# Performance work log

Hardware: AMD Instinct MI355X
Metric: run time of the kernel (lower is better)

## Reference

```python
import jax, jax.numpy as jnp
import numpy as np

INV_TEMP = 20.0
THRESHOLD = 0.01
SING_CUTOFF = 3.0
D0 = 128  # order-0 descriptor block
EPS = 1e-6


def setup_inputs() -> dict:
    key = jax.random.key(0)
    ks = jax.random.split(key, 6)
    B, N, M, D = 4, 4096, 4096, 256
    K = (D - D0) // 2
    return {
        "keypoints_A": jax.random.uniform(ks[0], (B, N, 2), jnp.float32) * 2.0 - 1.0,
        "descriptions_A": jax.random.normal(ks[1], (B, N, D), jnp.float32),
        "keypoints_B": jax.random.uniform(ks[2], (B, M, 2), jnp.float32) * 2.0 - 1.0,
        "descriptions_B": jax.random.normal(ks[3], (B, M, D), jnp.float32),
        "W_lstsq": jax.random.normal(ks[4], (D0, K), jnp.float32) * 0.1,
        "b_lstsq": jnp.zeros((K,), jnp.float32),
    }


def _svdvals_2x2(A):
    # singular values of [..,2,2] via eigenvalues of A^T A (closed form)
    M = jnp.einsum('...ki,...kj->...ij', A, A)
    t = M[..., 0, 0] + M[..., 1, 1]
    d = M[..., 0, 0] * M[..., 1, 1] - M[..., 0, 1] * M[..., 1, 0]
    disc = jnp.sqrt(jnp.maximum(0.25 * t * t - d, 0.0))
    lam_hi = 0.5 * t + disc
    lam_lo = jnp.maximum(0.5 * t - disc, 0.0)
    return jnp.sqrt(lam_hi), jnp.sqrt(lam_lo)


def reference(keypoints_A, descriptions_A, keypoints_B, descriptions_B, W_lstsq, b_lstsq):
    B, N, D = descriptions_A.shape
    K = (D - D0) // 2
    # --- dual softmax matcher (normalize=True) ---
    dA = descriptions_A / jnp.linalg.norm(descriptions_A, axis=-1, keepdims=True)
    dB = descriptions_B / jnp.linalg.norm(descriptions_B, axis=-1, keepdims=True)
    sim = INV_TEMP * jnp.einsum('bnd,bmd->bnm', dA, dB)  # [B,N,M]
    P = jax.nn.softmax(sim, axis=-2) * jax.nn.softmax(sim, axis=-1)
    # --- mutual nearest neighbors, fixed-shape (one candidate per A-row) ---
    j = jnp.argmax(P, axis=-1)  # [B,N]
    Pij = jnp.take_along_axis(P, j[..., None], axis=-1)[..., 0]
    colmax_j = jnp.take_along_axis(P.max(axis=-2), j, axis=-1)
    valid = (Pij >= colmax_j) & (Pij > THRESHOLD)  # mutual max + threshold
    # --- gather raw descriptors for matched pairs ---
    descB_m = jnp.take_along_axis(descriptions_B, j[..., None], axis=1)  # [B,N,D]
    desc0_A, desc1_A = descriptions_A[..., :D0], descriptions_A[..., D0:]
    desc0_B, desc1_B = descB_m[..., :D0], descB_m[..., D0:]
    # --- lstsq weights from order-0 features ---
    wA = jax.nn.softplus(desc0_A @ W_lstsq + b_lstsq)
    wB = jax.nn.softplus(desc0_B @ W_lstsq + b_lstsq)
    w = jnp.sqrt(wA * wB)  # [B,N,K]
    # --- weighted 2x2 affine lstsq: A x ~ y ---
    X = desc1_A.reshape(B, N, K, 2)
    Y = desc1_B.reshape(B, N, K, 2)
    G = jnp.einsum('bnk,bnki,bnkj->bnij', w, X, X) + EPS * jnp.eye(2, dtype=X.dtype)
    C = jnp.einsum('bnk,bnki,bnkj->bnij', w, Y, X)
    est = jnp.swapaxes(jnp.linalg.solve(G, jnp.swapaxes(C, -1, -2)), -1, -2)  # [B,N,2,2]
    # --- singular value / determinant filter ---
    s_hi, s_lo = _svdvals_2x2(est)
    good = jnp.isfinite(s_hi + s_lo) & (s_hi < SING_CUTOFF) & (s_lo > 1.0 / SING_CUTOFF)
    det = est[..., 0, 0] * est[..., 1, 1] - est[..., 0, 1] * est[..., 1, 0]
    good = good & (det > 0)  # remove_negative_determinants=True
    valid = valid & good
    matches_A = keypoints_A  # row i of A pairs with column j[b,i]
    matches_B = jnp.take_along_axis(keypoints_B, j[..., None], axis=1)
    return matches_A, matches_B, j, valid
```

## Files before the change

kernel.cpp:

```cpp
#include <hip/hip_runtime.h>
#include <math.h>

#define Bb   4
#define Nn   4096
#define Mm   4096
#define Dd   256
#define D0c  128
#define Kc   64

typedef _Float16 half8 __attribute__((ext_vector_type(8)));
typedef float    f32x4 __attribute__((ext_vector_type(4)));

__device__ __forceinline__ unsigned encf(float f) {
    unsigned u = __float_as_uint(f);
    return (u & 0x80000000u) ? ~u : (u | 0x80000000u);
}
__device__ __forceinline__ float decf(unsigned u) {
    return (u & 0x80000000u) ? __uint_as_float(u ^ 0x80000000u) : __uint_as_float(~u);
}
__device__ __forceinline__ float softplusf(float x) {
    return fmaxf(x, 0.f) + log1pf(expf(-fabsf(x)));
}
__device__ __forceinline__ void gl_lds16(const _Float16* g, _Float16* l) {
    __builtin_amdgcn_global_load_lds((const __attribute__((address_space(1))) void*)g,
                                     (__attribute__((address_space(3))) void*)l, 16, 0, 0);
}

__global__ __launch_bounds__(256) void prep_kernel(
    const float* __restrict__ dA, const float* __restrict__ dB,
    _Float16* __restrict__ Ah, _Float16* __restrict__ Al,
    _Float16* __restrict__ Bh, _Float16* __restrict__ Bl)
{
    const int t = threadIdx.x, wave = t >> 6, lane = t & 63;
    const int row = blockIdx.x * 4 + wave;
    const float* src = blockIdx.y ? dB : dA;
    _Float16* dh = blockIdx.y ? Bh : Ah;
    _Float16* dl = blockIdx.y ? Bl : Al;
    const float4 v = *(const float4*)&src[(size_t)row * Dd + lane * 4];
    float ss = v.x * v.x + v.y * v.y + v.z * v.z + v.w * v.w;
#pragma unroll
    for (int m = 32; m; m >>= 1) ss += __shfl_xor(ss, m, 64);
    const float inv = 1.0f / sqrtf(ss);
    float x[4] = {v.x * inv, v.y * inv, v.z * inv, v.w * inv};
    union { _Float16 h[4]; uint2 u; } ph, pl;
#pragma unroll
    for (int i = 0; i < 4; i++) {
        _Float16 h = (_Float16)x[i];
        ph.h[i] = h;
        pl.h[i] = (_Float16)((x[i] - (float)h) * 4096.f);
    }
    const size_t toff = (size_t)(row >> 7) * 32768
                      + (size_t)(lane >> 3) * 4096
                      + (size_t)((lane >> 1) & 3) * 1024
                      + (size_t)(row & 127) * 8 + (lane & 1) * 4;
    *(uint2*)&dh[toff] = ph.u;
    *(uint2*)&dl[toff] = pl.u;
}

template<int PB, int STORE>
__global__ __launch_bounds__(256, 2) void sim_kernel(
    const _Float16* __restrict__ Ah, const _Float16* __restrict__ Al,
    const _Float16* __restrict__ Bh, const _Float16* __restrict__ Bl,
    const float* __restrict__ Lrow_g, const float* __restrict__ Lcol_g,
    float* __restrict__ rowsumP, float* __restrict__ colsumP,
    float* __restrict__ rkey, int* __restrict__ rmArr, float* __restrict__ rcvArr,
    unsigned* __restrict__ cmU, float* __restrict__ simG, int b0)
{
    __shared__ _Float16 lds[2][4][4][128][8];
    __shared__ float    colp[128];
    __shared__ unsigned colu[128];
    __shared__ float    shL[128], shLc[128];

    const int t = threadIdx.x;
    const int wave = t >> 6, lane = t & 63;
    const int mt = blockIdx.x, nt = blockIdx.y, bbl = blockIdx.z;
    const int bb = b0 + bbl;
    const int n0 = nt * 128, m0 = mt * 128;

    if (PB) {
        if (t < 128) {
            shL[t]  = Lrow_g[bb * Nn + n0 + t];
            shLc[t] = Lcol_g[bb * Mm + m0 + t];
            colu[t] = 0u;
        }
    } else {
        if (t < 128) colp[t] = 0.f;
    }

    const _Float16* gb;
    {
        const size_t offA = (size_t)(bb * Nn + n0) * Dd;
        const size_t offB = (size_t)(bb * Mm + m0) * Dd;
        if      (wave == 0) gb = Ah + offA;
        else if (wave == 1) gb = Al + offA;
        else if (wave == 2) gb = Bh + offB;
        else                gb = Bl + offB;
    }

    f32x4 acc1[2][8], acc2[2][8];
#pragma unroll
    for (int ti = 0; ti < 2; ti++)
#pragma unroll
        for (int tj = 0; tj < 8; tj++) { acc1[ti][tj] = (f32x4)0.f; acc2[ti][tj] = (f32x4)0.f; }

    const int quad = lane >> 4, l15 = lane & 15;
    _Float16* lw0 = &lds[0][wave][0][0][0];
    _Float16* lw1 = &lds[1][wave][0][0][0];

#pragma unroll
    for (int q = 0; q < 8; ++q)
        gl_lds16(gb + q * 512 + lane * 8, lw0 + q * 512);

#pragma unroll
    for (int kc8 = 0; kc8 < 8; ++kc8) {
        const int cur = kc8 & 1;
        if (kc8 < 7) {
            _Float16* nw = cur ? lw0 : lw1;
            const _Float16* gsrc = gb + (kc8 + 1) * 4096;
#pragma unroll
            for (int q = 0; q < 8; ++q)
                gl_lds16(gsrc + q * 512 + lane * 8, nw + q * 512);
            asm volatile("s_waitcnt vmcnt(8)" ::: "memory");
        } else {
            asm volatile("s_waitcnt vmcnt(0)" ::: "memory");
        }
        __builtin_amdgcn_s_barrier();
        __builtin_amdgcn_sched_barrier(0);

        half8 afh[2], afl[2];
        afh[0] = *(const half8*)&lds[cur][0][quad][wave * 32 + l15][0];
        afh[1] = *(const half8*)&lds[cur][0][quad][wave * 32 + 16 + l15][0];
        afl[0] = *(const half8*)&lds[cur][1][quad][wave * 32 + l15][0];
        afl[1] = *(const half8*)&lds[cur][1][quad][wave * 32 + 16 + l15][0];
#pragma unroll
        for (int tj = 0; tj < 8; ++tj) {
            half8 bh = *(const half8*)&lds[cur][2][quad][tj * 16 + l15][0];
            half8 bl = *(const half8*)&lds[cur][3][quad][tj * 16 + l15][0];
#pragma unroll
            for (int ti = 0; ti < 2; ++ti) {
                acc1[ti][tj] = __builtin_amdgcn_mfma_f32_16x16x32_f16(afh[ti], bh, acc1[ti][tj], 0, 0, 0);
                acc2[ti][tj] = __builtin_amdgcn_mfma_f32_16x16x32_f16(afh[ti], bl, acc2[ti][tj], 0, 0, 0);
                acc2[ti][tj] = __builtin_amdgcn_mfma_f32_16x16x32_f16(afl[ti], bh, acc2[ti][tj], 0, 0, 0);
            }
        }
        asm volatile("s_waitcnt lgkmcnt(0)" ::: "memory");
        __builtin_amdgcn_s_barrier();
    }

    if (!PB) {
        float rp[8] = {0.f}, cp[8] = {0.f};
#pragma unroll
        for (int ti = 0; ti < 2; ++ti)
#pragma unroll
            for (int tj = 0; tj < 8; ++tj)
#pragma unroll
                for (int r = 0; r < 4; ++r) {
                    float dot = fmaf(acc2[ti][tj][r], 2.44140625e-4f, acc1[ti][tj][r]);
                    acc1[ti][tj][r] = dot;
                    float e = __expf(fmaf(20.f, dot, -20.f));
                    rp[ti * 4 + r] += e;
                    cp[tj] += e;
                }
#pragma unroll
        for (int i = 0; i < 8; ++i)
#pragma unroll
            for (int m = 1; m < 16; m <<= 1) rp[i] += __shfl_xor(rp[i], m, 64);
        if (l15 == 0) {
#pragma unroll
            for (int ti = 0; ti < 2; ++ti)
#pragma unroll
                for (int r = 0; r < 4; ++r)
                    rowsumP[(size_t)(bb * 32 + mt) * Nn + n0 + wave * 32 + ti * 16 + quad * 4 + r] = rp[ti * 4 + r];
        }
#pragma unroll
        for (int tj = 0; tj < 8; ++tj) {
            cp[tj] += __shfl_xor(cp[tj], 16, 64);
            cp[tj] += __shfl_xor(cp[tj], 32, 64);
        }
        if (quad == 0) {
#pragma unroll
            for (int tj = 0; tj < 8; ++tj) atomicAdd(&colp[tj * 16 + l15], cp[tj]);
        }
        __syncthreads();
        if (t < 128) colsumP[(size_t)(bb * 32 + nt) * Mm + m0 + t] = colp[t];
        if (STORE) {
            float* base = simG + ((size_t)bbl * Nn + n0) * Mm + m0;
#pragma unroll
            for (int ti = 0; ti < 2; ++ti)
#pragma unroll
                for (int r = 0; r < 4; ++r) {
                    float* rowp = base + (size_t)(wave * 32 + ti * 16 + quad * 4 + r) * Mm;
#pragma unroll
                    for (int tj = 0; tj < 8; ++tj)
                        __builtin_nontemporal_store(acc1[ti][tj][r], rowp + tj * 16 + l15);
                }
        }
    } else {
        float Lr[8];
#pragma unroll
        for (int ti = 0; ti < 2; ++ti)
#pragma unroll
            for (int r = 0; r < 4; ++r)
                Lr[ti * 4 + r] = shL[wave * 32 + ti * 16 + quad * 4 + r];

        float bk[8], bc[8];
        int bm[8];
        unsigned cu[8];
#pragma unroll
        for (int i = 0; i < 8; i++) { bk[i] = -INFINITY; bc[i] = -INFINITY; bm[i] = 0x7fffffff; }
#pragma unroll
        for (int j = 0; j < 8; j++) cu[j] = 0u;

#pragma unroll
        for (int ti = 0; ti < 2; ++ti)
#pragma unroll
            for (int tj = 0; tj < 8; ++tj)
#pragma unroll
                for (int r = 0; r < 4; ++r) {
                    float dot = fmaf(acc2[ti][tj][r], 2.44140625e-4f, acc1[ti][tj][r]);
                    float cv = fmaf(40.f, dot, -40.f - Lr[ti * 4 + r]);
                    float kv = cv - shLc[tj * 16 + l15];
                    const int i = ti * 4 + r;
                    if (kv > bk[i]) { bk[i] = kv; bm[i] = m0 + tj * 16 + l15; bc[i] = cv; }
                    unsigned e = encf(cv);
                    if (e > cu[tj]) cu[tj] = e;
                }
#pragma unroll
        for (int i = 0; i < 8; ++i) {
#pragma unroll
            for (int m = 1; m < 16; m <<= 1) {
                float okv = __shfl_xor(bk[i], m, 64);
                int   om  = __shfl_xor(bm[i], m, 64);
                float ocv = __shfl_xor(bc[i], m, 64);
                if (okv > bk[i] || (okv == bk[i] && om < bm[i])) { bk[i] = okv; bm[i] = om; bc[i] = ocv; }
            }
        }
        if (l15 == 0) {
#pragma unroll
            for (int ti = 0; ti < 2; ++ti)
#pragma unroll
                for (int r = 0; r < 4; ++r) {
                    const int i = ti * 4 + r;
                    size_t idx = (size_t)(bb * 32 + mt) * Nn + n0 + wave * 32 + ti * 16 + quad * 4 + r;
                    rkey[idx] = bk[i]; rmArr[idx] = bm[i]; rcvArr[idx] = bc[i];
                }
        }
#pragma unroll
        for (int tj = 0; tj < 8; ++tj) {
            unsigned o = __shfl_xor(cu[tj], 16, 64); if (o > cu[tj]) cu[tj] = o;
            o = __shfl_xor(cu[tj], 32, 64); if (o > cu[tj]) cu[tj] = o;
        }
        if (quad == 0) {
#pragma unroll
            for (int tj = 0; tj < 8; ++tj) atomicMax(&colu[tj * 16 + l15], cu[tj]);
        }
        __syncthreads();
        if (t < 128) cmU[(size_t)(bb * 32 + nt) * Mm + m0 + t] = colu[t];
    }
}

__global__ __launch_bounds__(256) void logsum_kernel(
    const float* __restrict__ rowsumP, const float* __restrict__ colsumP,
    float* __restrict__ Lrow, float* __restrict__ Lcol, int b0, int CB)
{
    int t = blockIdx.x * 256 + threadIdx.x;
    int half = CB * 4096;
    int which = t >= half;
    int idx = which ? (t - half) : t;
    int bb = b0 + (idx >> 12), n = idx & 4095;
    const float* P = which ? colsumP : rowsumP;
    float s = 0.f;
    for (int mt = 0; mt < 32; ++mt) s += P[(size_t)(bb * 32 + mt) * 4096 + n];
    (which ? Lcol : Lrow)[bb * 4096 + n] = logf(s);
}

__global__ __launch_bounds__(256) void scan_kernel(
    const float* __restrict__ simG,
    const float* __restrict__ Lrow, const float* __restrict__ Lcol,
    float* __restrict__ kvP, float* __restrict__ cvP, int* __restrict__ jP,
    unsigned* __restrict__ colPartU, int b0)
{
    __shared__ unsigned colu[1024];
    const int t = threadIdx.x, wave = t >> 6, lane = t & 63;
    const int blk = blockIdx.x;
    const int bbl = blk >> 9;
    const int r9 = blk & 511;
    const int stripe = r9 >> 2, q = r9 & 3;
    const int bb = b0 + bbl;
    const int col0 = q * 1024;
    const int row0 = stripe * 32 + wave * 8;

    for (int i = t; i < 1024; i += 256) colu[i] = 0u;
    __syncthreads();

    f32x4 Lc4[4], cmax[4];
    const float* LcB = Lcol + bb * Mm + col0;
#pragma unroll
    for (int c = 0; c < 4; ++c) {
        Lc4[c] = *(const f32x4*)&LcB[c * 256 + lane * 4];
        cmax[c] = (f32x4)(-INFINITY);
    }

    const float* rowbase = simG + (size_t)(bbl * Nn + row0) * Mm + col0;
    f32x4 cur[4], nxt[4];
#pragma unroll
    for (int c = 0; c < 4; ++c)
        cur[c] = __builtin_nontemporal_load((const f32x4*)&rowbase[c * 256 + lane * 4]);

    for (int r = 0; r < 8; ++r) {
        if (r < 7) {
            const float* nrow = rowbase + (size_t)(r + 1) * Mm;
#pragma unroll
            for (int c = 0; c < 4; ++c)
                nxt[c] = __builtin_nontemporal_load((const f32x4*)&nrow[c * 256 + lane * 4]);
        }
        const int n = bb * Nn + row0 + r;
        const float Ln = Lrow[n];
        const float cbias = -40.f - Ln;
        float bk = -INFINITY, bc = -INFINITY;
        int bm = 0x7fffffff;
#pragma unroll
        for (int c = 0; c < 4; ++c) {
            float cv0 = fmaf(40.f, cur[c].x, cbias);
            float cv1 = fmaf(40.f, cur[c].y, cbias);
            float cv2 = fmaf(40.f, cur[c].z, cbias);
            float cv3 = fmaf(40.f, cur[c].w, cbias);
            cmax[c].x = fmaxf(cmax[c].x, cv0);
            cmax[c].y = fmaxf(cmax[c].y, cv1);
            cmax[c].z = fmaxf(cmax[c].z, cv2);
            cmax[c].w = fmaxf(cmax[c].w, cv3);
            const int mb = col0 + c * 256 + lane * 4;
            float kv0 = cv0 - Lc4[c].x;
            float kv1 = cv1 - Lc4[c].y;
            float kv2 = cv2 - Lc4[c].z;
            float kv3 = cv3 - Lc4[c].w;
            if (kv0 > bk) { bk = kv0; bm = mb;     bc = cv0; }
            if (kv1 > bk) { bk = kv1; bm = mb + 1; bc = cv1; }
            if (kv2 > bk) { bk = kv2; bm = mb + 2; bc = cv2; }
            if (kv3 > bk) { bk = kv3; bm = mb + 3; bc = cv3; }
        }
#pragma unroll
        for (int sh = 1; sh < 64; sh <<= 1) {
            float okv = __shfl_xor(bk, sh, 64);
            int   om  = __shfl_xor(bm, sh, 64);
            float ocv = __shfl_xor(bc, sh, 64);
            if (okv > bk || (okv == bk && om < bm)) { bk = okv; bm = om; bc = ocv; }
        }
        if (lane == 0) {
            size_t o = ((size_t)bb * Nn + row0 + r) * 4 + q;
            kvP[o] = bk; cvP[o] = bc; jP[o] = bm;
        }
#pragma unroll
        for (int c = 0; c < 4; ++c) cur[c] = nxt[c];
    }
#pragma unroll
    for (int c = 0; c < 4; ++c) {
        const int mb = c * 256 + lane * 4;
        atomicMax(&colu[mb],     encf(cmax[c].x));
        atomicMax(&colu[mb + 1], encf(cmax[c].y));
        atomicMax(&colu[mb + 2], encf(cmax[c].z));
        atomicMax(&colu[mb + 3], encf(cmax[c].w));
    }
    __syncthreads();
    unsigned* cp = colPartU + (size_t)blk * 1024;
    for (int i = t; i < 1024; i += 256) cp[i] = colu[i];
}

__global__ __launch_bounds__(256) void colreduce_kernel(
    const unsigned* __restrict__ colPartU, float* __restrict__ colMaxF, int b0)
{
    const int tid = blockIdx.x * 256 + threadIdx.x;
    const int bbl = tid >> 12;
    const int m = tid & 4095;
    const int q = m >> 10, ml = m & 1023;
    unsigned mx = 0u;
    for (int s = 0; s < 128; ++s) {
        unsigned v = colPartU[((size_t)(bbl * 512 + s * 4 + q)) * 1024 + ml];
        if (v > mx) mx = v;
    }
    colMaxF[(size_t)(b0 + bbl) * Mm + m] = decf(mx);
}

__global__ __launch_bounds__(256) void validate_kernel(
    const float* __restrict__ kvP, const float* __restrict__ cvP,
    const int* __restrict__ jP, const float* __restrict__ colMaxF,
    float* __restrict__ outJ, int* __restrict__ jIdx, int* __restrict__ v1)
{
    const float LOG_THR = -4.605170185988091f;
    const int p = blockIdx.x * 256 + threadIdx.x;
    const int bb = p >> 12;
    float bk = -INFINITY, bc = -INFINITY;
    int bm = 0x7fffffff;
#pragma unroll
    for (int q = 0; q < 4; ++q) {
        size_t o = (size_t)p * 4 + q;
        float k = kvP[o];
        int   m = jP[o];
        if (k > bk || (k == bk && m < bm)) { bk = k; bm = m; bc = cvP[o]; }
    }
    const float cm = colMaxF[(size_t)bb * Mm + bm];
    const int ok = (bk > LOG_THR) && (bc >= cm);
    outJ[p] = (float)bm;
    jIdx[p] = bm;
    v1[p] = ok;
}

__global__ __launch_bounds__(256) void finalize_kernel(
    const float* __restrict__ rkey, const int* __restrict__ rmArr,
    const float* __restrict__ rcvArr, const unsigned* __restrict__ cmU,
    float* __restrict__ outJ, int* __restrict__ jIdx, int* __restrict__ v1)
{
    const float LOG_THR = -4.605170185988091f;
    int p = blockIdx.x * 256 + threadIdx.x;
    int bb = p >> 12, n = p & 4095;
    float bk = -INFINITY, bc = -INFINITY;
    int bm = 0;
    for (int mt = 0; mt < 32; ++mt) {
        size_t idx = (size_t)(bb * 32 + mt) * Nn + n;
        float k = rkey[idx];
        if (k > bk) { bk = k; bm = rmArr[idx]; bc = rcvArr[idx]; }
    }
    unsigned u = 0u;
    for (int nt = 0; nt < 32; ++nt) {
        unsigned c = cmU[(size_t)(bb * 32 + nt) * Mm + bm];
        if (c > u) u = c;
    }
    float cm = decf(u);
    int ok = (bk > LOG_THR) && (bc >= cm);
    outJ[p] = (float)bm;
    jIdx[p] = bm;
    v1[p]   = ok;
}

__global__ __launch_bounds__(256) void affine_kernel(
    const float* __restrict__ descA, const float* __restrict__ descB,
    const float* __restrict__ kpA, const float* __restrict__ kpB,
    const float* __restrict__ W, const float* __restrict__ bvec,
    const int* __restrict__ jIdx, const int* __restrict__ v1,
    float* __restrict__ outA, float* __restrict__ outB, float* __restrict__ outV)
{
    __shared__ float Ws[D0c * Kc];
    __shared__ float sbuf[4][4][D0c];
    const int t = threadIdx.x, wave = t >> 6, lane = t & 63;
    for (int i = t; i < D0c * Kc; i += 256) Ws[i] = W[i];
    const float bl = bvec[lane];
    __syncthreads();

    float* s0A = sbuf[wave][0];
    float* s1A = sbuf[wave][1];
    float* s0B = sbuf[wave][2];
    float* s1B = sbuf[wave][3];

    for (int p = 0; p < 8; ++p) {
        const int point = blockIdx.x * 32 + wave * 8 + p;
        const int bb = point >> 12;
        const int j = jIdx[point];
        const float* da = descA + (size_t)point * Dd;
        const float* db = descB + (size_t)(bb * Mm + j) * Dd;
        s0A[lane] = da[lane];       s0A[64 + lane] = da[64 + lane];
        s1A[lane] = da[128 + lane]; s1A[64 + lane] = da[192 + lane];
        s0B[lane] = db[lane];       s0B[64 + lane] = db[64 + lane];
        s1B[lane] = db[128 + lane]; s1B[64 + lane] = db[192 + lane];
        __syncthreads();

        float xa = bl, xb = bl;
#pragma unroll 8
        for (int d = 0; d < 128; ++d) {
            float w_ = Ws[d * 64 + lane];
            xa = fmaf(s0A[d], w_, xa);
            xb = fmaf(s0B[d], w_, xb);
        }
        float wa = softplusf(xa), wb = softplusf(xb);
        float w = sqrtf(wa * wb);
        float x0 = s1A[2 * lane], x1 = s1A[2 * lane + 1];
        float y0 = s1B[2 * lane], y1 = s1B[2 * lane + 1];
        float g00 = w * x0 * x0, g01 = w * x0 * x1, g11 = w * x1 * x1;
        float c00 = w * y0 * x0, c01 = w * y0 * x1;
        float c10 = w * y1 * x0, c11 = w * y1 * x1;
#pragma unroll
        for (int m = 32; m; m >>= 1) {
            g00 += __shfl_xor(g00, m, 64); g01 += __shfl_xor(g01, m, 64); g11 += __shfl_xor(g11, m, 64);
            c00 += __shfl_xor(c00, m, 64); c01 += __shfl_xor(c01, m, 64);
            c10 += __shfl_xor(c10, m, 64); c11 += __shfl_xor(c11, m, 64);
        }
        if (lane == 0) {
            g00 += 1e-6f; g11 += 1e-6f;
            float det = g00 * g11 - g01 * g01;
            float e00 = (c00 * g11 - c01 * g01) / det;
            float e01 = (c01 * g00 - c00 * g01) / det;
            float e10 = (c10 * g11 - c11 * g01) / det;
            float e11 = (c11 * g00 - c10 * g01) / det;
            float m00 = e00 * e00 + e10 * e10;
            float m01 = e00 * e01 + e10 * e11;
            float m11 = e01 * e01 + e11 * e11;
            float tr = m00 + m11;
            float dm = m00 * m11 - m01 * m01;
            float disc = sqrtf(fmaxf(0.25f * tr * tr - dm, 0.f));
            float lhi = 0.5f * tr + disc;
            float llo = fmaxf(0.5f * tr - disc, 0.f);
            float shi = sqrtf(lhi), slo = sqrtf(llo);
            float sdet = e00 * e11 - e01 * e10;
            int good = isfinite(shi + slo) && (shi < 3.0f) && (slo > 0.33333334f) && (sdet > 0.f);
            int valid = v1[point] && good;
            outA[2 * point]     = kpA[2 * point];
            outA[2 * point + 1] = kpA[2 * point + 1];
            const float* kb = kpB + (size_t)(bb * Mm + j) * 2;
            outB[2 * point]     = kb[0];
            outB[2 * point + 1] = kb[1];
            outV[point] = valid ? 1.f : 0.f;
        }
        __syncthreads();
    }
}

extern "C" void kernel_launch(void* const* d_in, const int* in_sizes, int n_in,
                              void* d_out, int out_size, void* d_ws, size_t ws_size,
                              hipStream_t stream) {
    const float* kpA = (const float*)d_in[0];
    const float* dA  = (const float*)d_in[1];
    const float* kpB = (const float*)d_in[2];
    const float* dB  = (const float*)d_in[3];
    const float* W   = (const float*)d_in[4];
    const float* bl  = (const float*)d_in[5];
    float* out = (float*)d_out;

    char* ws = (char*)d_ws;
    _Float16* Ah = (_Float16*)ws;  ws += 8388608;
    _Float16* Al = (_Float16*)ws;  ws += 8388608;
    _Float16* Bh = (_Float16*)ws;  ws += 8388608;
    _Float16* Bl = (_Float16*)ws;  ws += 8388608;
    float*    rowsumP = (float*)ws;    ws += 2097152;
    float*    colsumP = (float*)ws;    ws += 2097152;
    float*    Lrow    = (float*)ws;    ws += 65536;
    float*    Lcol    = (float*)ws;    ws += 65536;
    int*      jIdx    = (int*)ws;      ws += 65536;
    int*      v1      = (int*)ws;      ws += 65536;
    float*    kvP     = (float*)ws;    ws += 262144;
    float*    cvP     = (float*)ws;    ws += 262144;
    int*      jP      = (int*)ws;      ws += 262144;
    float*    colMaxF = (float*)ws;    ws += 65536;
    char*     big     = ws;

    const size_t base = (size_t)(big - (char*)d_ws);

    float*    rkey  = (float*)big;
    int*      rmArr = (int*)(big + 2097152);
    float*    rcvArr= (float*)(big + 4194304);
    unsigned* cmU   = (unsigned*)(big + 6291456);

    float* outA = out;
    float* outB = out + 32768;
    float* outJ = out + 65536;
    float* outV = out + 81920;

    const size_t per = 67108864ull + 2097152ull;
    int CB = 0;
    if      (ws_size >= base + 2 * per) CB = 2;
    else if (ws_size >= base + 1 * per) CB = 1;

    prep_kernel<<<dim3(4096, 2), 256, 0, stream>>>(dA, dB, Ah, Al, Bh, Bl);

    if (CB) {
        float*    simG     = (float*)big;
        unsigned* colPartU = (unsigned*)(big + (size_t)CB * 67108864);
        for (int b0 = 0; b0 < Bb; b0 += CB) {
            sim_kernel<0, 1><<<dim3(32, 32, CB), 256, 0, stream>>>(
                Ah, Al, Bh, Bl, nullptr, nullptr, rowsumP, colsumP,
                nullptr, nullptr, nullptr, nullptr, simG, b0);
            logsum_kernel<<<32 * CB, 256, 0, stream>>>(rowsumP, colsumP, Lrow, Lcol, b0, CB);
            scan_kernel<<<512 * CB, 256, 0, stream>>>(simG, Lrow, Lcol, kvP, cvP, jP, colPartU, b0);
            colreduce_kernel<<<16 * CB, 256, 0, stream>>>(colPartU, colMaxF, b0);
        }
        validate_kernel<<<64, 256, 0, stream>>>(kvP, cvP, jP, colMaxF, outJ, jIdx, v1);
    } else {
        sim_kernel<0, 0><<<dim3(32, 32, Bb), 256, 0, stream>>>(
            Ah, Al, Bh, Bl, nullptr, nullptr, rowsumP, colsumP,
            nullptr, nullptr, nullptr, nullptr, nullptr, 0);
        logsum_kernel<<<32 * Bb, 256, 0, stream>>>(rowsumP, colsumP, Lrow, Lcol, 0, Bb);
        sim_kernel<1, 0><<<dim3(32, 32, Bb), 256, 0, stream>>>(
            Ah, Al, Bh, Bl, Lrow, Lcol, nullptr, nullptr,
            rkey, rmArr, rcvArr, cmU, nullptr, 0);
        finalize_kernel<<<64, 256, 0, stream>>>(rkey, rmArr, rcvArr, cmU, outJ, jIdx, v1);
    }
    affine_kernel<<<512, 256, 0, stream>>>(dA, dB, kpA, kpB, W, bl, jIdx, v1, outA, outB, outV);
}
```

Before: 347.2 us.

## Fold column-max reduction into scan via global atomics and drop nontemporal hints

Removes the separate colreduce kernel and its partial-max buffer: each scan block now atomically maxes its shared-memory column maxima straight into a global colMaxU array, which prep_kernel zero-initializes and validate decodes. It also switches the simG stores and loads from nontemporal to regular accesses, so the freshly written similarity tile can stay in cache for the scan pass. The cost is global atomic contention (128 blocks per column group) in exchange for one fewer launch and less traffic. Regular stores may pollute cache for other data.

Result: faster. 331.1 us (-4.6%).

```diff
diff --git a/kernel.cpp b/kernel.cpp
--- a/kernel.cpp
+++ b/kernel.cpp
@@ -29,10 +29,12 @@
 __global__ __launch_bounds__(256) void prep_kernel(
     const float* __restrict__ dA, const float* __restrict__ dB,
     _Float16* __restrict__ Ah, _Float16* __restrict__ Al,
-    _Float16* __restrict__ Bh, _Float16* __restrict__ Bl)
+    _Float16* __restrict__ Bh, _Float16* __restrict__ Bl,
+    unsigned* __restrict__ colMaxU)
 {
     const int t = threadIdx.x, wave = t >> 6, lane = t & 63;
     const int row = blockIdx.x * 4 + wave;
+    if (blockIdx.y == 0 && lane == 0) colMaxU[row] = 0u;
     const float* src = blockIdx.y ? dB : dA;
     _Float16* dh = blockIdx.y ? Bh : Ah;
     _Float16* dl = blockIdx.y ? Bl : Al;
@@ -192,7 +194,7 @@
                     float* rowp = base + (size_t)(wave * 32 + ti * 16 + quad * 4 + r) * Mm;
 #pragma unroll
                     for (int tj = 0; tj < 8; ++tj)
-                        __builtin_nontemporal_store(acc1[ti][tj][r], rowp + tj * 16 + l15);
+                        rowp[tj * 16 + l15] = acc1[ti][tj][r];
                 }
         }
     } else {
@@ -278,7 +280,7 @@
     const float* __restrict__ simG,
     const float* __restrict__ Lrow, const float* __restrict__ Lcol,
     float* __restrict__ kvP, float* __restrict__ cvP, int* __restrict__ jP,
-    unsigned* __restrict__ colPartU, int b0)
+    unsigned* __restrict__ colMaxU, int b0)
 {
     __shared__ unsigned colu[1024];
     const int t = threadIdx.x, wave = t >> 6, lane = t & 63;
@@ -305,14 +307,14 @@
     f32x4 cur[4], nxt[4];
 #pragma unroll
     for (int c = 0; c < 4; ++c)
-        cur[c] = __builtin_nontemporal_load((const f32x4*)&rowbase[c * 256 + lane * 4]);
+        cur[c] = *(const f32x4*)&rowbase[c * 256 + lane * 4];
 
     for (int r = 0; r < 8; ++r) {
         if (r < 7) {
             const float* nrow = rowbase + (size_t)(r + 1) * Mm;
 #pragma unroll
             for (int c = 0; c < 4; ++c)
-                nxt[c] = __builtin_nontemporal_load((const f32x4*)&nrow[c * 256 + lane * 4]);
+                nxt[c] = *(const f32x4*)&nrow[c * 256 + lane * 4];
         }
         const int n = bb * Nn + row0 + r;
         const float Ln = Lrow[n];
@@ -362,28 +364,13 @@
         atomicMax(&colu[mb + 3], encf(cmax[c].w));
     }
     __syncthreads();
-    unsigned* cp = colPartU + (size_t)blk * 1024;
-    for (int i = t; i < 1024; i += 256) cp[i] = colu[i];
-}
-
-__global__ __launch_bounds__(256) void colreduce_kernel(
-    const unsigned* __restrict__ colPartU, float* __restrict__ colMaxF, int b0)
-{
-    const int tid = blockIdx.x * 256 + threadIdx.x;
-    const int bbl = tid >> 12;
-    const int m = tid & 4095;
-    const int q = m >> 10, ml = m & 1023;
-    unsigned mx = 0u;
-    for (int s = 0; s < 128; ++s) {
-        unsigned v = colPartU[((size_t)(bbl * 512 + s * 4 + q)) * 1024 + ml];
-        if (v > mx) mx = v;
-    }
-    colMaxF[(size_t)(b0 + bbl) * Mm + m] = decf(mx);
+    unsigned* cm = colMaxU + (size_t)bb * Mm + col0;
+    for (int i = t; i < 1024; i += 256) atomicMax(&cm[i], colu[i]);
 }
 
 __global__ __launch_bounds__(256) void validate_kernel(
     const float* __restrict__ kvP, const float* __restrict__ cvP,
-    const int* __restrict__ jP, const float* __restrict__ colMaxF,
+    const int* __restrict__ jP, const unsigned* __restrict__ colMaxU,
     float* __restrict__ outJ, int* __restrict__ jIdx, int* __restrict__ v1)
 {
     const float LOG_THR = -4.605170185988091f;
@@ -398,7 +385,7 @@
         int   m = jP[o];
         if (k > bk || (k == bk && m < bm)) { bk = k; bm = m; bc = cvP[o]; }
     }
-    const float cm = colMaxF[(size_t)bb * Mm + bm];
+    const float cm = decf(colMaxU[(size_t)bb * Mm + bm]);
     const int ok = (bk > LOG_THR) && (bc >= cm);
     outJ[p] = (float)bm;
     jIdx[p] = bm;
@@ -538,7 +525,7 @@
     float*    kvP     = (float*)ws;    ws += 262144;
     float*    cvP     = (float*)ws;    ws += 262144;
     int*      jP      = (int*)ws;      ws += 262144;
-    float*    colMaxF = (float*)ws;    ws += 65536;
+    unsigned* colMaxU = (unsigned*)ws; ws += 65536;
     char*     big     = ws;
 
     const size_t base = (size_t)(big - (char*)d_ws);
@@ -553,25 +540,23 @@
     float* outJ = out + 65536;
     float* outV = out + 81920;
 
-    const size_t per = 67108864ull + 2097152ull;
+    const size_t per = 67108864ull;
     int CB = 0;
     if      (ws_size >= base + 2 * per) CB = 2;
     else if (ws_size >= base + 1 * per) CB = 1;
 
-    prep_kernel<<<dim3(4096, 2), 256, 0, stream>>>(dA, dB, Ah, Al, Bh, Bl);
+    prep_kernel<<<dim3(4096, 2), 256, 0, stream>>>(dA, dB, Ah, Al, Bh, Bl, colMaxU);
 
     if (CB) {
-        float*    simG     = (float*)big;
-        unsigned* colPartU = (unsigned*)(big + (size_t)CB * 67108864);
+        float* simG = (float*)big;
         for (int b0 = 0; b0 < Bb; b0 += CB) {
             sim_kernel<0, 1><<<dim3(32, 32, CB), 256, 0, stream>>>(
                 Ah, Al, Bh, Bl, nullptr, nullptr, rowsumP, colsumP,
                 nullptr, nullptr, nullptr, nullptr, simG, b0);
             logsum_kernel<<<32 * CB, 256, 0, stream>>>(rowsumP, colsumP, Lrow, Lcol, b0, CB);
-            scan_kernel<<<512 * CB, 256, 0, stream>>>(simG, Lrow, Lcol, kvP, cvP, jP, colPartU, b0);
-            colreduce_kernel<<<16 * CB, 256, 0, stream>>>(colPartU, colMaxF, b0);
-        }
-        validate_kernel<<<64, 256, 0, stream>>>(kvP, cvP, jP, colMaxF, outJ, jIdx, v1);
+            scan_kernel<<<512 * CB, 256, 0, stream>>>(simG, Lrow, Lcol, kvP, cvP, jP, colMaxU, b0);
+        }
+        validate_kernel<<<64, 256, 0, stream>>>(kvP, cvP, jP, colMaxU, outJ, jIdx, v1);
     } else {
         sim_kernel<0, 0><<<dim3(32, 32, Bb), 256, 0, stream>>>(
             Ah, Al, Bh, Bl, nullptr, nullptr, rowsumP, colsumP,
```
